# Performance work log

Measured on AMD Instinct MI355X. Metric: run time of the kernel, lower is better.

## Reference

```python
import jax, jax.numpy as jnp
import numpy as np

B, S, N, H, D = 8, 2048, 8, 1024, 64  # batch, seq, n_tasks, hidden, dense_size
T = 50.0  # temperature (fusion_config['temperature']=True)


def setup_inputs() -> dict:
    key = jax.random.key(0)
    ks = jax.random.split(key, 10)
    return {
        "query": jax.random.normal(ks[0], (B, S, H), dtype=jnp.float32),
        "key": jax.random.normal(ks[1], (B, S, N, D), dtype=jnp.float32),
        "value": jax.random.normal(ks[2], (B, S, N, H), dtype=jnp.float32),
        "attention_mask": jax.random.randint(ks[3], (B, S), 0, 2, dtype=jnp.int32),
        # nn.Linear weights are [out, in]
        "Wq": jax.random.normal(ks[4], (D, H), dtype=jnp.float32) * 0.02,
        "bq": jnp.zeros((D,), dtype=jnp.float32),
        "Wk": jax.random.normal(ks[5], (D, D), dtype=jnp.float32) * 0.02,
        "bk": jnp.zeros((D,), dtype=jnp.float32),
        "Wv": jax.random.normal(ks[6], (H, H), dtype=jnp.float32) * 0.02,
        "bv": jnp.zeros((H,), dtype=jnp.float32),
    }


def reference(query, key, value, attention_mask, Wq, bq, Wk, bk, Wv, bv):
    # mask==0 means valid token (per original: (attention_mask == 0).float())
    mask = (attention_mask == 0).astype(jnp.float32)          # [B, S]
    length = jnp.sum(mask, axis=1)                            # [B]
    # masked mean pooling (instead of repeat-based broadcasting)
    key_sent = jnp.einsum("bs,bsnd->bnd", mask, key) / length[:, None, None]   # [B, N, D]
    query_sent = jnp.einsum("bs,bsh->bh", mask, query) / length[:, None]       # [B, H]
    query_enc = query_sent @ Wq.T + bq                        # [B, D]
    key_enc = key_sent @ Wk.T + bk                            # [B, N, D]
    value_enc = jnp.einsum("bsnh,oh->bsno", value, Wv) + bv   # [B, S, N, H]
    scores = jnp.einsum("bnd,bd->bn", key_enc, query_enc)     # [B, N]
    probs = jax.nn.softmax(scores / T, axis=-1)               # [B, N]
    result = jnp.einsum("bn,bsnh->bsh", probs, value_enc)     # [B, S, H]
    return result
```

## Files before the change

### kernel.cpp

```cpp
#include <hip/hip_runtime.h>
#include <hip/hip_bf16.h>
#include <stdint.h>

#define BB 8
#define SS 2048
#define NTASK 8
#define HH 1024
#define DD 64
#define TEMP 50.0f

typedef __attribute__((ext_vector_type(8))) short short8;
typedef __attribute__((ext_vector_type(4))) float floatx4;

static __device__ __forceinline__ unsigned short f2bf(float f) {
  union { float f; unsigned int u; } v; v.f = f;
  unsigned int u = v.u;
  unsigned int r = u + 0x7FFFu + ((u >> 16) & 1u);
  return (unsigned short)(r >> 16);
}

#define SCHUNKS 64
#define SCHUNK (SS / SCHUNKS)

__global__ void pool_kernel(const float* __restrict__ query,
                            const float* __restrict__ key,
                            const int* __restrict__ amask,
                            const float* __restrict__ Wv,
                            float* __restrict__ qsum,
                            float* __restrict__ ksum,
                            float* __restrict__ lensum,
                            unsigned short* __restrict__ WvB)
{
  __shared__ float valid[SCHUNK];
  int b = blockIdx.x >> 6;
  int chunk = blockIdx.x & 63;
  int s0 = chunk * SCHUNK;
  int tid = threadIdx.x;
  if (tid < SCHUNK) valid[tid] = (amask[b * SS + s0 + tid] == 0) ? 1.0f : 0.0f;
  __syncthreads();

  {
    size_t i = ((size_t)blockIdx.x * 256 + tid) * 8;
    floatx4 v0 = *(const floatx4*)(Wv + i);
    floatx4 v1 = *(const floatx4*)(Wv + i + 4);
    union { unsigned short us[8]; uint4 u4; } pk;
    pk.us[0] = f2bf(v0.x); pk.us[1] = f2bf(v0.y);
    pk.us[2] = f2bf(v0.z); pk.us[3] = f2bf(v0.w);
    pk.us[4] = f2bf(v1.x); pk.us[5] = f2bf(v1.y);
    pk.us[6] = f2bf(v1.z); pk.us[7] = f2bf(v1.w);
    *(uint4*)(WvB + i) = pk.u4;
  }

  {
    const float* qb = query + ((size_t)b * SS + s0) * HH;
    int h0 = tid * 4;
    floatx4 acc = {0.f, 0.f, 0.f, 0.f};
    for (int s = 0; s < SCHUNK; ++s) {
      if (valid[s] != 0.0f) {
        floatx4 v = *(const floatx4*)(qb + (size_t)s * HH + h0);
        acc += v;
      }
    }
    atomicAdd(&qsum[b * HH + h0 + 0], acc.x);
    atomicAdd(&qsum[b * HH + h0 + 1], acc.y);
    atomicAdd(&qsum[b * HH + h0 + 2], acc.z);
    atomicAdd(&qsum[b * HH + h0 + 3], acc.w);
  }
  if (tid < 128) {
    const float* kb = key + ((size_t)b * SS + s0) * (NTASK * DD);
    int i0 = tid * 4;
    floatx4 acc = {0.f, 0.f, 0.f, 0.f};
    for (int s = 0; s < SCHUNK; ++s) {
      if (valid[s] != 0.0f) {
        floatx4 v = *(const floatx4*)(kb + (size_t)s * (NTASK * DD) + i0);
        acc += v;
      }
    }
    atomicAdd(&ksum[b * NTASK * DD + i0 + 0], acc.x);
    atomicAdd(&ksum[b * NTASK * DD + i0 + 1], acc.y);
    atomicAdd(&ksum[b * NTASK * DD + i0 + 2], acc.z);
    atomicAdd(&ksum[b * NTASK * DD + i0 + 3], acc.w);
  }
  if (tid == 0) {
    float c = 0.f;
    for (int s = 0; s < SCHUNK; ++s) c += valid[s];
    atomicAdd(&lensum[b], c);
  }
}

__global__ void qenc_kernel(const float* __restrict__ qsum,
                            const float* __restrict__ lensum,
                            const float* __restrict__ Wq,
                            const float* __restrict__ bq,
                            float* __restrict__ qe)
{
  int b = blockIdx.x >> 6;
  int d = blockIdx.x & 63;
  int tid = threadIdx.x;
  const float* wr = Wq + (size_t)d * HH;
  const float* qs = qsum + (size_t)b * HH;
  float acc = 0.f;
  for (int h = tid; h < HH; h += 256) acc += qs[h] * wr[h];
  __shared__ float red[256];
  red[tid] = acc;
  __syncthreads();
  for (int off = 128; off > 0; off >>= 1) {
    if (tid < off) red[tid] += red[tid + off];
    __syncthreads();
  }
  if (tid == 0) qe[blockIdx.x] = red[0] / lensum[b] + bq[d];
}

__global__ void probs_kernel(const float* __restrict__ ksum,
                             const float* __restrict__ lensum,
                             const float* __restrict__ qe_g,
                             const float* __restrict__ Wk,
                             const float* __restrict__ bk,
                             float* __restrict__ probs)
{
  __shared__ float ke[BB * NTASK * DD];
  __shared__ float qe[BB * DD];
  __shared__ float sc[BB * NTASK];
  int tid = threadIdx.x;
  for (int i = tid; i < BB * DD; i += 256) qe[i] = qe_g[i];
  for (int idx = tid; idx < BB * NTASK * DD; idx += 256) {
    int d = idx & 63;
    int bn = idx >> 6;
    int b = bn >> 3;
    const float* wr = Wk + d * DD;
    const float* ks = ksum + bn * DD;
    float acc = 0.f;
#pragma unroll 8
    for (int d2 = 0; d2 < DD; ++d2) acc += ks[d2] * wr[d2];
    ke[idx] = acc / lensum[b] + bk[d];
  }
  __syncthreads();
  if (tid < BB * NTASK) {
    int b = tid >> 3;
    float acc = 0.f;
    for (int d = 0; d < DD; ++d) acc += ke[tid * DD + d] * qe[b * DD + d];
    sc[tid] = acc / TEMP;
  }
  __syncthreads();
  if (tid < BB * NTASK) {
    int b = tid >> 3;
    float mx = -1e30f;
    for (int n = 0; n < NTASK; ++n) mx = fmaxf(mx, sc[b * NTASK + n]);
    float den = 0.f;
    for (int n = 0; n < NTASK; ++n) den += expf(sc[b * NTASK + n] - mx);
    probs[tid] = expf(sc[tid] - mx) / den;
  }
}

#define VROWS 8
__global__ void vmix_kernel(const float* __restrict__ value,
                            const float* __restrict__ probs,
                            unsigned short* __restrict__ vmix)
{
  __shared__ float p[NTASK];
  int bs0 = blockIdx.x * VROWS;
  int b = bs0 >> 11;
  if (threadIdx.x < NTASK) p[threadIdx.x] = probs[b * NTASK + threadIdx.x];
  __syncthreads();
  int h0 = threadIdx.x * 4;
  for (int r = 0; r < VROWS; ++r) {
    const float* vp = value + (size_t)(bs0 + r) * NTASK * HH;
    floatx4 acc = {0.f, 0.f, 0.f, 0.f};
#pragma unroll
    for (int n = 0; n < NTASK; ++n) {
      floatx4 v = __builtin_nontemporal_load(
          (const floatx4*)(vp + (size_t)n * HH + h0));
      acc += p[n] * v;
    }
    union { unsigned short us[4]; uint2 u2; } pk;
    pk.us[0] = f2bf(acc.x);
    pk.us[1] = f2bf(acc.y);
    pk.us[2] = f2bf(acc.z);
    pk.us[3] = f2bf(acc.w);
    *(uint2*)(vmix + (size_t)(bs0 + r) * HH + h0) = pk.u2;
  }
}

#define BM 128
#define BN 128
#define BK 32

#define GLDS16(gsrc, ldst)                                                     \
  __builtin_amdgcn_global_load_lds(                                           \
      (const __attribute__((address_space(1))) void*)(gsrc),                   \
      (__attribute__((address_space(3))) void*)(ldst), 16, 0, 0)

__global__ __launch_bounds__(256)
void gemm_kernel(const unsigned short* __restrict__ A,
                 const unsigned short* __restrict__ Bm,
                 const float* __restrict__ bv,
                 float* __restrict__ C)
{
  const int N = HH;
  const int K = HH;
  __shared__ unsigned short As[BM * BK];
  __shared__ unsigned short Bs[BN * BK];

  int tid = threadIdx.x;
  int bflat = (int)blockIdx.x;
  int xcd = bflat & 7;
  int j = bflat >> 3;
  int ytile = j & 7;
  int xtile = xcd + ((j >> 3) << 3);
  int m0 = xtile * BM;
  int n0 = ytile * BN;
  int wave = tid >> 6;
  int lane = tid & 63;
  int wr = wave >> 1, wc = wave & 1;
  int quad = lane >> 4;
  int l16 = lane & 15;

  floatx4 acc[4][4] = {};

  int srow = wave * 32 + (lane >> 2);
  int schk = (lane & 3) * 8;
  const unsigned short* ga0 = A  + (size_t)(m0 + srow) * K + schk;
  const unsigned short* ga1 = ga0 + (size_t)16 * K;
  const unsigned short* gb0 = Bm + (size_t)(n0 + srow) * K + schk;
  const unsigned short* gb1 = gb0 + (size_t)16 * K;
  unsigned short* la0 = As + (wave * 32) * BK;
  unsigned short* la1 = As + (wave * 32 + 16) * BK;
  unsigned short* lb0 = Bs + (wave * 32) * BK;
  unsigned short* lb1 = Bs + (wave * 32 + 16) * BK;

  const int NKB = K / BK;
  for (int kb = 0; kb < NKB; ++kb) {
    int ko = kb * BK;
    GLDS16(ga0 + ko, la0);
    GLDS16(ga1 + ko, la1);
    GLDS16(gb0 + ko, lb0);
    GLDS16(gb1 + ko, lb1);
    __syncthreads();

    short8 af[4], bf[4];
#pragma unroll
    for (int mi = 0; mi < 4; ++mi)
      af[mi] = *(const short8*)&As[(wr * 64 + mi * 16 + l16) * BK + quad * 8];
#pragma unroll
    for (int ni = 0; ni < 4; ++ni)
      bf[ni] = *(const short8*)&Bs[(wc * 64 + ni * 16 + l16) * BK + quad * 8];
#pragma unroll
    for (int mi = 0; mi < 4; ++mi)
#pragma unroll
      for (int ni = 0; ni < 4; ++ni)
        acc[mi][ni] = __builtin_amdgcn_mfma_f32_16x16x32_bf16(
            af[mi], bf[ni], acc[mi][ni], 0, 0, 0);
    __syncthreads();
  }

#pragma unroll
  for (int ni = 0; ni < 4; ++ni) {
    int gn = n0 + wc * 64 + ni * 16 + l16;
    float bvv = bv[gn];
#pragma unroll
    for (int mi = 0; mi < 4; ++mi) {
      int gm = m0 + wr * 64 + mi * 16 + quad * 4;
#pragma unroll
      for (int r = 0; r < 4; ++r)
        __builtin_nontemporal_store(acc[mi][ni][r] + bvv,
                                    &C[(size_t)(gm + r) * N + gn]);
    }
  }
}

extern "C" void kernel_launch(void* const* d_in, const int* in_sizes, int n_in,
                              void* d_out, int out_size, void* d_ws, size_t ws_size,
                              hipStream_t stream) {
  const float* query = (const float*)d_in[0];
  const float* key   = (const float*)d_in[1];
  const float* value = (const float*)d_in[2];
  const int*   amask = (const int*)d_in[3];
  const float* Wq = (const float*)d_in[4];
  const float* bq = (const float*)d_in[5];
  const float* Wk = (const float*)d_in[6];
  const float* bk = (const float*)d_in[7];
  const float* Wv = (const float*)d_in[8];
  const float* bv = (const float*)d_in[9];
  float* out = (float*)d_out;

  char* ws = (char*)d_ws;
  unsigned short* vmix = (unsigned short*)(ws);
  unsigned short* WvB  = (unsigned short*)(ws + (size_t)33554432);
  float* qsum   = (float*)(ws + (size_t)35651584);
  float* ksum   = qsum + BB * HH;
  float* lensum = ksum + BB * NTASK * DD;
  float* probs  = lensum + BB;
  float* qe     = probs + BB * NTASK;

  hipMemsetAsync(qsum, 0, (size_t)(BB * HH + BB * NTASK * DD + BB) * sizeof(float), stream);

  pool_kernel<<<BB * SCHUNKS, 256, 0, stream>>>(query, key, amask, Wv, qsum, ksum, lensum, WvB);
  qenc_kernel<<<BB * DD, 256, 0, stream>>>(qsum, lensum, Wq, bq, qe);
  probs_kernel<<<1, 256, 0, stream>>>(ksum, lensum, qe, Wk, bk, probs);
  vmix_kernel<<<BB * SS / VROWS, 256, 0, stream>>>(value, probs, vmix);
  gemm_kernel<<<1024, 256, 0, stream>>>(vmix, WvB, bv, out);
}
```

Measured before the change: 857.0 us.

## Fuse probability-weighted value mixing into GEMM A-tile producer with double buffering

Removes the separate vmix kernel and its bf16 intermediate buffer. The GEMM now reads fp32 value directly, mixes the 8 tasks with probs in registers, converts to bf16 and writes the A tile into LDS. Each block covers 64 rows against the full 1024-wide N with 512 threads, and A and B tiles are double-buffered in LDS. This saves a 32MB write and read round trip and one launch. In exchange, each block reloads all of Wv (2MB bf16, L2-resident), uses 256 blocks with larger per-block LDS and register use, and some latency may become exposed.

New measurement: 850.7 us. Within noise of the previous version (-0.7%).

```diff
diff --git a/kernel.cpp b/kernel.cpp
--- a/kernel.cpp
+++ b/kernel.cpp
@@ -152,118 +152,133 @@
   }
 }
 
-#define VROWS 8
-__global__ void vmix_kernel(const float* __restrict__ value,
-                            const float* __restrict__ probs,
-                            unsigned short* __restrict__ vmix)
-{
-  __shared__ float p[NTASK];
-  int bs0 = blockIdx.x * VROWS;
-  int b = bs0 >> 11;
-  if (threadIdx.x < NTASK) p[threadIdx.x] = probs[b * NTASK + threadIdx.x];
-  __syncthreads();
-  int h0 = threadIdx.x * 4;
-  for (int r = 0; r < VROWS; ++r) {
-    const float* vp = value + (size_t)(bs0 + r) * NTASK * HH;
-    floatx4 acc = {0.f, 0.f, 0.f, 0.f};
-#pragma unroll
-    for (int n = 0; n < NTASK; ++n) {
-      floatx4 v = __builtin_nontemporal_load(
-          (const floatx4*)(vp + (size_t)n * HH + h0));
-      acc += p[n] * v;
-    }
-    union { unsigned short us[4]; uint2 u2; } pk;
-    pk.us[0] = f2bf(acc.x);
-    pk.us[1] = f2bf(acc.y);
-    pk.us[2] = f2bf(acc.z);
-    pk.us[3] = f2bf(acc.w);
-    *(uint2*)(vmix + (size_t)(bs0 + r) * HH + h0) = pk.u2;
-  }
-}
-
-#define BM 128
-#define BN 128
-#define BK 32
+#define BMF 64
+#define BKF 32
 
 #define GLDS16(gsrc, ldst)                                                     \
   __builtin_amdgcn_global_load_lds(                                           \
       (const __attribute__((address_space(1))) void*)(gsrc),                   \
       (__attribute__((address_space(3))) void*)(ldst), 16, 0, 0)
 
-__global__ __launch_bounds__(256)
-void gemm_kernel(const unsigned short* __restrict__ A,
-                 const unsigned short* __restrict__ Bm,
-                 const float* __restrict__ bv,
-                 float* __restrict__ C)
+__global__ __launch_bounds__(512)
+void fused_gemm_kernel(const float* __restrict__ value,
+                       const unsigned short* __restrict__ Bm,
+                       const float* __restrict__ probs,
+                       const float* __restrict__ bv,
+                       float* __restrict__ C)
 {
-  const int N = HH;
-  const int K = HH;
-  __shared__ unsigned short As[BM * BK];
-  __shared__ unsigned short Bs[BN * BK];
-
-  int tid = threadIdx.x;
-  int bflat = (int)blockIdx.x;
-  int xcd = bflat & 7;
-  int j = bflat >> 3;
-  int ytile = j & 7;
-  int xtile = xcd + ((j >> 3) << 3);
-  int m0 = xtile * BM;
-  int n0 = ytile * BN;
-  int wave = tid >> 6;
-  int lane = tid & 63;
-  int wr = wave >> 1, wc = wave & 1;
-  int quad = lane >> 4;
-  int l16 = lane & 15;
-
-  floatx4 acc[4][4] = {};
-
-  int srow = wave * 32 + (lane >> 2);
-  int schk = (lane & 3) * 8;
-  const unsigned short* ga0 = A  + (size_t)(m0 + srow) * K + schk;
-  const unsigned short* ga1 = ga0 + (size_t)16 * K;
-  const unsigned short* gb0 = Bm + (size_t)(n0 + srow) * K + schk;
-  const unsigned short* gb1 = gb0 + (size_t)16 * K;
-  unsigned short* la0 = As + (wave * 32) * BK;
-  unsigned short* la1 = As + (wave * 32 + 16) * BK;
-  unsigned short* lb0 = Bs + (wave * 32) * BK;
-  unsigned short* lb1 = Bs + (wave * 32 + 16) * BK;
-
-  const int NKB = K / BK;
-  for (int kb = 0; kb < NKB; ++kb) {
-    int ko = kb * BK;
-    GLDS16(ga0 + ko, la0);
-    GLDS16(ga1 + ko, la1);
-    GLDS16(gb0 + ko, lb0);
-    GLDS16(gb1 + ko, lb1);
+  __shared__ unsigned short As[2][BMF * BKF];
+  __shared__ unsigned short Bs[2][HH * BKF];
+
+  const int tid = threadIdx.x;
+  const int wave = tid >> 6;
+  const int lane = tid & 63;
+  const int quad = lane >> 4;
+  const int l16 = lane & 15;
+  const int bs0 = (int)blockIdx.x * BMF;
+  const int b = bs0 >> 11;
+
+  float p[NTASK];
+#pragma unroll
+  for (int n = 0; n < NTASK; ++n) p[n] = probs[b * NTASK + n];
+
+  const int ar = tid >> 3;
+  const int akq = (tid & 7) * 4;
+  const float* vrow = value + (size_t)(bs0 + ar) * (NTASK * HH) + akq;
+  const int awr = ar * BKF + akq;
+
+  const int brow = wave * 128 + (lane >> 2);
+  const int bchk = (lane & 3) * 8;
+  const unsigned short* gB = Bm + (size_t)brow * HH + bchk;
+
+  floatx4 acc[4][8] = {};
+  floatx4 v[NTASK];
+
+#pragma unroll
+  for (int n = 0; n < NTASK; ++n)
+    v[n] = __builtin_nontemporal_load((const floatx4*)(vrow + (size_t)n * HH));
+#pragma unroll
+  for (int c = 0; c < 8; ++c)
+    GLDS16(gB + (size_t)(c * 16) * HH, &Bs[0][(wave * 128 + c * 16) * BKF]);
+  {
+    floatx4 m = {0.f, 0.f, 0.f, 0.f};
+#pragma unroll
+    for (int n = 0; n < NTASK; ++n) m += p[n] * v[n];
+    union { unsigned short us[4]; uint2 u2; } pk;
+    pk.us[0] = f2bf(m.x); pk.us[1] = f2bf(m.y);
+    pk.us[2] = f2bf(m.z); pk.us[3] = f2bf(m.w);
+    *(uint2*)&As[0][awr] = pk.u2;
+  }
+  __syncthreads();
+
+  int cur = 0;
+  for (int kb = 0; kb < 31; ++kb) {
+    const int nxt = cur ^ 1;
+    const int ko = (kb + 1) * BKF;
+
+#pragma unroll
+    for (int n = 0; n < NTASK; ++n)
+      v[n] = __builtin_nontemporal_load(
+          (const floatx4*)(vrow + (size_t)n * HH + ko));
+#pragma unroll
+    for (int c = 0; c < 8; ++c)
+      GLDS16(gB + (size_t)(c * 16) * HH + ko,
+             &Bs[nxt][(wave * 128 + c * 16) * BKF]);
+
+    short8 af[4];
+#pragma unroll
+    for (int mi = 0; mi < 4; ++mi)
+      af[mi] = *(const short8*)&As[cur][(mi * 16 + l16) * BKF + quad * 8];
+#pragma unroll
+    for (int ni = 0; ni < 8; ++ni) {
+      short8 bf = *(const short8*)
+          &Bs[cur][(wave * 128 + ni * 16 + l16) * BKF + quad * 8];
+#pragma unroll
+      for (int mi = 0; mi < 4; ++mi)
+        acc[mi][ni] = __builtin_amdgcn_mfma_f32_16x16x32_bf16(
+            af[mi], bf, acc[mi][ni], 0, 0, 0);
+    }
+
+    {
+      floatx4 m = {0.f, 0.f, 0.f, 0.f};
+#pragma unroll
+      for (int n = 0; n < NTASK; ++n) m += p[n] * v[n];
+      union { unsigned short us[4]; uint2 u2; } pk;
+      pk.us[0] = f2bf(m.x); pk.us[1] = f2bf(m.y);
+      pk.us[2] = f2bf(m.z); pk.us[3] = f2bf(m.w);
+      *(uint2*)&As[nxt][awr] = pk.u2;
+    }
     __syncthreads();
-
-    short8 af[4], bf[4];
+    cur = nxt;
+  }
+
+  {
+    short8 af[4];
 #pragma unroll
     for (int mi = 0; mi < 4; ++mi)
-      af[mi] = *(const short8*)&As[(wr * 64 + mi * 16 + l16) * BK + quad * 8];
-#pragma unroll
-    for (int ni = 0; ni < 4; ++ni)
-      bf[ni] = *(const short8*)&Bs[(wc * 64 + ni * 16 + l16) * BK + quad * 8];
-#pragma unroll
-    for (int mi = 0; mi < 4; ++mi)
-#pragma unroll
-      for (int ni = 0; ni < 4; ++ni)
+      af[mi] = *(const short8*)&As[cur][(mi * 16 + l16) * BKF + quad * 8];
+#pragma unroll
+    for (int ni = 0; ni < 8; ++ni) {
+      short8 bf = *(const short8*)
+          &Bs[cur][(wave * 128 + ni * 16 + l16) * BKF + quad * 8];
+#pragma unroll
+      for (int mi = 0; mi < 4; ++mi)
         acc[mi][ni] = __builtin_amdgcn_mfma_f32_16x16x32_bf16(
-            af[mi], bf[ni], acc[mi][ni], 0, 0, 0);
-    __syncthreads();
-  }
-
-#pragma unroll
-  for (int ni = 0; ni < 4; ++ni) {
-    int gn = n0 + wc * 64 + ni * 16 + l16;
+            af[mi], bf, acc[mi][ni], 0, 0, 0);
+    }
+  }
+
+#pragma unroll
+  for (int ni = 0; ni < 8; ++ni) {
+    int gn = wave * 128 + ni * 16 + l16;
     float bvv = bv[gn];
 #pragma unroll
     for (int mi = 0; mi < 4; ++mi) {
-      int gm = m0 + wr * 64 + mi * 16 + quad * 4;
+      int gm = bs0 + mi * 16 + quad * 4;
 #pragma unroll
       for (int r = 0; r < 4; ++r)
         __builtin_nontemporal_store(acc[mi][ni][r] + bvv,
-                                    &C[(size_t)(gm + r) * N + gn]);
+                                    &C[(size_t)(gm + r) * HH + gn]);
     }
   }
 }
@@ -284,9 +299,8 @@
   float* out = (float*)d_out;
 
   char* ws = (char*)d_ws;
-  unsigned short* vmix = (unsigned short*)(ws);
-  unsigned short* WvB  = (unsigned short*)(ws + (size_t)33554432);
-  float* qsum   = (float*)(ws + (size_t)35651584);
+  unsigned short* WvB = (unsigned short*)(ws);
+  float* qsum   = (float*)(ws + (size_t)2097152);
   float* ksum   = qsum + BB * HH;
   float* lensum = ksum + BB * NTASK * DD;
   float* probs  = lensum + BB;
@@ -297,6 +311,5 @@
   pool_kernel<<<BB * SCHUNKS, 256, 0, stream>>>(query, key, amask, Wv, qsum, ksum, lensum, WvB);
   qenc_kernel<<<BB * DD, 256, 0, stream>>>(qsum, lensum, Wq, bq, qe);
   probs_kernel<<<1, 256, 0, stream>>>(ksum, lensum, qe, Wk, bk, probs);
-  vmix_kernel<<<BB * SS / VROWS, 256, 0, stream>>>(value, probs, vmix);
-  gemm_kernel<<<1024, 256, 0, stream>>>(vmix, WvB, bv, out);
-}
+  fused_gemm_kernel<<<BB * SS / BMF, 512, 0, stream>>>(value, WvB, probs, bv, out);
+}
```
